# Kernel tuning notes

Measured on AMD Instinct MI355X. Metric: run time of the kernel, lower is better.

Reference implementation:

```python
import jax, jax.numpy as jnp
import numpy as np

H = 32        # query heads
KV = 8        # kv heads (GQA)
D = 128       # head_dim
HID = 4096    # hidden_size
T = 2048      # tokens (single causal sequence)
THETA = 10000.0


def setup_inputs() -> dict:
    key = jax.random.key(0)
    k1, k2, k3 = jax.random.split(key, 3)
    return {
        "positions": jnp.arange(T, dtype=jnp.int32),
        "hidden_states": jax.random.normal(k1, (T, HID), dtype=jnp.float32),
        "w_qkv": jax.random.normal(k2, ((H + 2 * KV) * D, HID), dtype=jnp.float32) * 0.02,
        "w_o": jax.random.normal(k3, (HID, H * D), dtype=jnp.float32) * 0.02,
    }


def _rope_neox(x, cos, sin):
    # x: [T, h, D]; cos/sin: [T, D/2]
    half = x.shape[-1] // 2
    x1, x2 = x[..., :half], x[..., half:]
    c, s = cos[:, None, :], sin[:, None, :]
    return jnp.concatenate([x1 * c - x2 * s, x2 * c + x1 * s], axis=-1)


def reference(positions, hidden_states, w_qkv, w_o):
    t = hidden_states.shape[0]
    qkv = hidden_states @ w_qkv.T                      # [T, (H+2KV)*D]
    q, k, v = jnp.split(qkv, [H * D, H * D + KV * D], axis=-1)
    q = q.reshape(t, H, D)
    k = k.reshape(t, KV, D)
    v = v.reshape(t, KV, D)

    # neox-style RoPE over full head_dim
    half = D // 2
    inv_freq = 1.0 / (THETA ** (jnp.arange(0, D, 2, dtype=jnp.float32) / D))  # [D/2]
    freqs = positions.astype(jnp.float32)[:, None] * inv_freq                 # [T, D/2]
    cos, sin = jnp.cos(freqs), jnp.sin(freqs)
    q = _rope_neox(q, cos, sin)
    k = _rope_neox(k, cos, sin)

    # GQA: expand kv heads to match query heads
    rep = H // KV
    k = jnp.repeat(k, rep, axis=1)                     # [T, H, D]
    v = jnp.repeat(v, rep, axis=1)

    scale = D ** -0.5
    scores = jnp.einsum('thd,shd->hts', q, k) * scale  # [H, T, T]
    causal = positions[:, None] >= positions[None, :]  # [T, T]
    neg = jnp.finfo(scores.dtype).min
    scores = jnp.where(causal[None], scores, neg)
    attn = jax.nn.softmax(scores, axis=-1)
    out = jnp.einsum('hts,shd->thd', attn, v).reshape(t, H * D)
    return out @ w_o.T                                 # [T, HID]
```

## Files before the change

### kernel.cpp

```cpp
#include <hip/hip_runtime.h>
#include <hip/hip_bf16.h>
#include <cstdint>

typedef __bf16 bf16;
typedef __bf16 bf16x8 __attribute__((ext_vector_type(8)));
typedef float f32x4 __attribute__((ext_vector_type(4)));

#define DEV __device__ __forceinline__

DEV f32x4 mfma16(bf16x8 a, bf16x8 b, f32x4 c) {
  return __builtin_amdgcn_mfma_f32_16x16x32_bf16(a, b, c, 0, 0, 0);
}

DEV void gl2lds16(const void* g, void* l) {
  __builtin_amdgcn_global_load_lds((__attribute__((address_space(1))) void*)g,
                                   (__attribute__((address_space(3))) void*)l,
                                   16, 0, 0);
}

DEV void cvt8(const float* __restrict__ s, bf16* __restrict__ d) {
  f32x4 a = *(const f32x4*)(s);
  f32x4 b = *(const f32x4*)(s + 4);
  bf16x8 o;
#pragma unroll
  for (int e = 0; e < 4; ++e) { o[e] = (bf16)a[e]; o[e + 4] = (bf16)b[e]; }
  *(bf16x8*)(d) = o;
}

__global__ void cvt3(const float* __restrict__ s0, bf16* __restrict__ d0, int n0,
                     const float* __restrict__ s1, bf16* __restrict__ d1, int n1,
                     const float* __restrict__ s2, bf16* __restrict__ d2) {
  long i = ((long)blockIdx.x * 256 + threadIdx.x) * 8;
  if (i < n0) { cvt8(s0 + i, d0 + i); return; }
  i -= n0;
  if (i < n1) { cvt8(s1 + i, d1 + i); return; }
  i -= n1;
  cvt8(s2 + i, d2 + i);
}

template <typename OutT>
__global__ __launch_bounds__(256) void gemm_bt(const bf16* __restrict__ A,
                                               const bf16* __restrict__ B,
                                               OutT* __restrict__ C,
                                               int M, int N, int K) {
  __shared__ bf16 As[128 * 32];
  __shared__ bf16 Bs[128 * 32];
  const int tid = threadIdx.x;
  const int lane = tid & 63, w = tid >> 6;
  const int wm = w & 1, wn = w >> 1;
  const int quad = lane >> 4, r = lane & 15;
  const long mBase = (long)blockIdx.y * 128, nBase = (long)blockIdx.x * 128;
  f32x4 acc[4][4];
#pragma unroll
  for (int i = 0; i < 4; ++i)
#pragma unroll
    for (int j = 0; j < 4; ++j) acc[i][j] = f32x4{0.f, 0.f, 0.f, 0.f};

  for (int k0 = 0; k0 < K; k0 += 32) {
    __syncthreads();
#pragma unroll
    for (int j = 0; j < 2; ++j) {
      const int c = w * 128 + j * 64 + lane;
      const int row = c >> 2, kc = c & 3;
      const int kcx = kc ^ (row & 3);
      gl2lds16(A + (mBase + row) * (long)K + k0 + kcx * 8,
               (char*)As + (w * 128 + j * 64) * 16);
      gl2lds16(B + (nBase + row) * (long)K + k0 + kcx * 8,
               (char*)Bs + (w * 128 + j * 64) * 16);
    }
    __syncthreads();
    bf16x8 af[4], bfr[4];
#pragma unroll
    for (int i = 0; i < 4; ++i) {
      af[i]  = *(const bf16x8*)(&As[(wm * 64 + i * 16 + r) * 32 + ((quad ^ (r & 3)) << 3)]);
      bfr[i] = *(const bf16x8*)(&Bs[(wn * 64 + i * 16 + r) * 32 + ((quad ^ (r & 3)) << 3)]);
    }
#pragma unroll
    for (int mi = 0; mi < 4; ++mi)
#pragma unroll
      for (int ni = 0; ni < 4; ++ni)
        acc[mi][ni] = mfma16(af[mi], bfr[ni], acc[mi][ni]);
  }
#pragma unroll
  for (int mi = 0; mi < 4; ++mi)
#pragma unroll
    for (int ni = 0; ni < 4; ++ni)
#pragma unroll
      for (int rg = 0; rg < 4; ++rg) {
        long row = mBase + wm * 64 + mi * 16 + quad * 4 + rg;
        long col = nBase + wn * 64 + ni * 16 + r;
        C[row * N + col] = (OutT)acc[mi][ni][rg];
      }
}

__global__ void rope_kernel(bf16* __restrict__ qkv, const int* __restrict__ pos) {
  int idx = blockIdx.x * 256 + threadIdx.x;
  int g = idx & 7;
  int rest = idx >> 3;
  int head = rest % 40;
  int t = rest / 40;
  bf16* p = qkv + (long)t * 6144 + head * 128 + g * 8;
  bf16x8 a = *(const bf16x8*)(p);
  bf16x8 b = *(const bf16x8*)(p + 64);
  const float pf = (float)pos[t];
  bf16x8 oa, ob;
#pragma unroll
  for (int e = 0; e < 8; ++e) {
    const int d = g * 8 + e;
    const float invf = __builtin_expf(-(float)d * (9.210340371976184f / 64.0f));
    const float fr = pf * invf;
    const float c = __builtin_cosf(fr), s = __builtin_sinf(fr);
    const float x1 = (float)a[e], x2 = (float)b[e];
    oa[e] = (bf16)(x1 * c - x2 * s);
    ob[e] = (bf16)(x2 * c + x1 * s);
  }
  *(bf16x8*)(p) = oa;
  *(bf16x8*)(p + 64) = ob;
}

__global__ __launch_bounds__(256, 2) void attn_kernel(const bf16* __restrict__ qkv,
                                                      bf16* __restrict__ out) {
  constexpr int LDV = 72, LDP = 72;
  constexpr float SCL2 = 0.08838834764831845f * 1.4426950408889634f;
  __shared__ bf16 Ks[64 * 128];
  __shared__ bf16 Vt[128 * LDV];
  __shared__ bf16 Ps[64 * LDP];
  const int tid = threadIdx.x;
  const int lane = tid & 63, w = tid >> 6;
  const int quad = lane >> 4, r = lane & 15;
  const int pr = blockIdx.x, h = blockIdx.y;
  const int kvh = h >> 2;

  bf16x8 kreg[4], vreg[4];
  int srow[4], sdc[4];
#pragma unroll
  for (int ii = 0; ii < 4; ++ii) {
    const int c = ii * 256 + tid;
    srow[ii] = c >> 4;
    sdc[ii] = c & 15;
  }

  for (int which = 0; which < 2; ++which) {
    const int qt = which ? (31 - pr) : pr;
    const int rowq = qt * 64 + w * 16;

    bf16x8 qf[4];
#pragma unroll
    for (int ks = 0; ks < 4; ++ks)
      qf[ks] = *(const bf16x8*)(qkv + (long)(rowq + r) * 6144 + h * 128 + ks * 32 + quad * 8);

    f32x4 of[8];
#pragma unroll
    for (int di = 0; di < 8; ++di) of[di] = f32x4{0.f, 0.f, 0.f, 0.f};
    float mrun[4], lrun[4];
#pragma unroll
    for (int rg = 0; rg < 4; ++rg) { mrun[rg] = -__builtin_inff(); lrun[rg] = 0.f; }

    const int ntiles = qt + 1;
#pragma unroll
    for (int ii = 0; ii < 4; ++ii) {
      const long rb = (long)srow[ii] * 6144 + kvh * 128;
      kreg[ii] = *(const bf16x8*)(qkv + rb + 4096 + sdc[ii] * 8);
      vreg[ii] = *(const bf16x8*)(qkv + rb + 5120 + sdc[ii] * 8);
    }

    for (int kt = 0; kt < ntiles; ++kt) {
      const int kvbase = kt * 64;
      __syncthreads();
#pragma unroll
      for (int ii = 0; ii < 4; ++ii) {
        const int row = srow[ii], dc = sdc[ii];
        *(bf16x8*)(&Ks[row * 128 + ((dc ^ (row & 15)) << 3)]) = kreg[ii];
        const int pc = (((row >> 3) ^ (dc & 7)) << 3) + (row & 7);
#pragma unroll
        for (int e = 0; e < 8; ++e) Vt[(dc * 8 + e) * LDV + pc] = vreg[ii][e];
      }
      __syncthreads();
      {
        const int kvn = (kt + 1 < ntiles) ? (kt + 1) * 64 : kt * 64;
#pragma unroll
        for (int ii = 0; ii < 4; ++ii) {
          const long rb = (long)(kvn + srow[ii]) * 6144 + kvh * 128;
          kreg[ii] = *(const bf16x8*)(qkv + rb + 4096 + sdc[ii] * 8);
          vreg[ii] = *(const bf16x8*)(qkv + rb + 5120 + sdc[ii] * 8);
        }
      }

      f32x4 sacc[4];
#pragma unroll
      for (int ni = 0; ni < 4; ++ni) sacc[ni] = f32x4{0.f, 0.f, 0.f, 0.f};
#pragma unroll
      for (int ks = 0; ks < 4; ++ks) {
        bf16x8 kf[4];
#pragma unroll
        for (int ni = 0; ni < 4; ++ni)
          kf[ni] = *(const bf16x8*)(&Ks[(ni * 16 + r) * 128 + (((ks * 4 + quad) ^ r) << 3)]);
#pragma unroll
        for (int ni = 0; ni < 4; ++ni) sacc[ni] = mfma16(qf[ks], kf[ni], sacc[ni]);
      }

      float mt[4];
#pragma unroll
      for (int rg = 0; rg < 4; ++rg) mt[rg] = -1e30f;
      if (kt == qt) {
        const int rq = rowq + quad * 4;
#pragma unroll
        for (int ni = 0; ni < 4; ++ni) {
          const int ck = kvbase + ni * 16 + r;
#pragma unroll
          for (int rg = 0; rg < 4; ++rg) {
            float sv = sacc[ni][rg];
            sv = (ck > rq + rg) ? -1e30f : sv;
            sacc[ni][rg] = sv;
            mt[rg] = fmaxf(mt[rg], sv);
          }
        }
      } else {
#pragma unroll
        for (int ni = 0; ni < 4; ++ni)
#pragma unroll
          for (int rg = 0; rg < 4; ++rg) mt[rg] = fmaxf(mt[rg], sacc[ni][rg]);
      }
#pragma unroll
      for (int rg = 0; rg < 4; ++rg) {
        float v = mt[rg];
        v = fmaxf(v, __shfl_xor(v, 1));
        v = fmaxf(v, __shfl_xor(v, 2));
        v = fmaxf(v, __shfl_xor(v, 4));
        v = fmaxf(v, __shfl_xor(v, 8));
        mt[rg] = v;
      }
      float alpha[4], rsum[4];
#pragma unroll
      for (int rg = 0; rg < 4; ++rg) {
        const float mnew = fmaxf(mrun[rg], mt[rg]);
        alpha[rg] = __builtin_exp2f((mrun[rg] - mnew) * SCL2);
        mrun[rg] = mnew;
        rsum[rg] = 0.f;
      }
#pragma unroll
      for (int ni = 0; ni < 4; ++ni)
#pragma unroll
        for (int rg = 0; rg < 4; ++rg) {
          const float pv = __builtin_exp2f((sacc[ni][rg] - mrun[rg]) * SCL2);
          rsum[rg] += pv;
          Ps[(w * 16 + quad * 4 + rg) * LDP + ni * 16 + r] = (bf16)pv;
        }
#pragma unroll
      for (int rg = 0; rg < 4; ++rg) {
        float v = rsum[rg];
        v += __shfl_xor(v, 1);
        v += __shfl_xor(v, 2);
        v += __shfl_xor(v, 4);
        v += __shfl_xor(v, 8);
        lrun[rg] = lrun[rg] * alpha[rg] + v;
      }
#pragma unroll
      for (int di = 0; di < 8; ++di)
#pragma unroll
        for (int rg = 0; rg < 4; ++rg) of[di][rg] *= alpha[rg];

#pragma unroll
      for (int js = 0; js < 2; ++js) {
        const bf16x8 pf = *(const bf16x8*)(&Ps[(w * 16 + r) * LDP + js * 32 + quad * 8]);
#pragma unroll
        for (int di = 0; di < 8; ++di) {
          const int vrow = di * 16 + r;
          const int vcol = (((js * 4 + quad) ^ ((vrow >> 3) & 7)) << 3);
          const bf16x8 vf = *(const bf16x8*)(&Vt[vrow * LDV + vcol]);
          of[di] = mfma16(pf, vf, of[di]);
        }
      }
    }

#pragma unroll
    for (int rg = 0; rg < 4; ++rg) {
      const float inv = 1.f / lrun[rg];
      const long t = rowq + quad * 4 + rg;
#pragma unroll
      for (int di = 0; di < 8; ++di)
        out[t * 4096 + h * 128 + di * 16 + r] = (bf16)(of[di][rg] * inv);
    }
  }
}

extern "C" void kernel_launch(void* const* d_in, const int* in_sizes, int n_in,
                              void* d_out, int out_size, void* d_ws, size_t ws_size,
                              hipStream_t stream) {
  const int* positions = (const int*)d_in[0];
  const float* hidden = (const float*)d_in[1];
  const float* w_qkv = (const float*)d_in[2];
  const float* w_o = (const float*)d_in[3];
  float* out = (float*)d_out;

  char* ws = (char*)d_ws;
  bf16* hid_b  = (bf16*)(ws);
  bf16* wqkv_b = (bf16*)(ws + 16777216);
  bf16* wo_b   = (bf16*)(ws + 67108864);
  bf16* qkv    = (bf16*)(ws + 100663296);
  bf16* attn   = (bf16*)(ws + 125829120);

  cvt3<<<24576, 256, 0, stream>>>(hidden, hid_b, 8388608,
                                  w_qkv, wqkv_b, 25165824,
                                  w_o, wo_b);
  gemm_bt<bf16><<<dim3(48, 16), 256, 0, stream>>>(hid_b, wqkv_b, qkv, 2048, 6144, 4096);
  rope_kernel<<<2560, 256, 0, stream>>>(qkv, positions);
  attn_kernel<<<dim3(16, 32), 256, 0, stream>>>(qkv, attn);
  gemm_bt<float><<<dim3(32, 16), 256, 0, stream>>>(attn, wo_b, out, 2048, 4096, 4096);
}
```

Before: 573.4 us.

## Split-K output GEMM with atomics, double-buffer attention K/V, drop GEMM LDS swizzle

The output projection GEMM is split along K into two halves across blockIdx.z, accumulating with float atomicAdd into a zeroed output, to double the block count. The attention kernel double-buffers K and V in LDS, removing one barrier per tile. The GEMM's XOR swizzle on LDS loads and reads is removed, which may add bank conflicts. The atomics add a memset and nondeterministic summation order.

```diff
diff --git a/kernel.cpp b/kernel.cpp
--- a/kernel.cpp
+++ b/kernel.cpp
@@ -38,7 +38,7 @@
   cvt8(s2 + i, d2 + i);
 }
 
-template <typename OutT>
+template <typename OutT, int SPLIT>
 __global__ __launch_bounds__(256) void gemm_bt(const bf16* __restrict__ A,
                                                const bf16* __restrict__ B,
                                                OutT* __restrict__ C,
@@ -50,30 +50,31 @@
   const int wm = w & 1, wn = w >> 1;
   const int quad = lane >> 4, r = lane & 15;
   const long mBase = (long)blockIdx.y * 128, nBase = (long)blockIdx.x * 128;
+  const int Kh = K / SPLIT;
+  const int kBeg = blockIdx.z * Kh, kEnd = kBeg + Kh;
   f32x4 acc[4][4];
 #pragma unroll
   for (int i = 0; i < 4; ++i)
 #pragma unroll
     for (int j = 0; j < 4; ++j) acc[i][j] = f32x4{0.f, 0.f, 0.f, 0.f};
 
-  for (int k0 = 0; k0 < K; k0 += 32) {
+  for (int k0 = kBeg; k0 < kEnd; k0 += 32) {
     __syncthreads();
 #pragma unroll
     for (int j = 0; j < 2; ++j) {
       const int c = w * 128 + j * 64 + lane;
       const int row = c >> 2, kc = c & 3;
-      const int kcx = kc ^ (row & 3);
-      gl2lds16(A + (mBase + row) * (long)K + k0 + kcx * 8,
+      gl2lds16(A + (mBase + row) * (long)K + k0 + kc * 8,
                (char*)As + (w * 128 + j * 64) * 16);
-      gl2lds16(B + (nBase + row) * (long)K + k0 + kcx * 8,
+      gl2lds16(B + (nBase + row) * (long)K + k0 + kc * 8,
                (char*)Bs + (w * 128 + j * 64) * 16);
     }
     __syncthreads();
     bf16x8 af[4], bfr[4];
 #pragma unroll
     for (int i = 0; i < 4; ++i) {
-      af[i]  = *(const bf16x8*)(&As[(wm * 64 + i * 16 + r) * 32 + ((quad ^ (r & 3)) << 3)]);
-      bfr[i] = *(const bf16x8*)(&Bs[(wn * 64 + i * 16 + r) * 32 + ((quad ^ (r & 3)) << 3)]);
+      af[i]  = *(const bf16x8*)(&As[(wm * 64 + i * 16 + r) * 32 + quad * 8]);
+      bfr[i] = *(const bf16x8*)(&Bs[(wn * 64 + i * 16 + r) * 32 + quad * 8]);
     }
 #pragma unroll
     for (int mi = 0; mi < 4; ++mi)
@@ -89,7 +90,10 @@
       for (int rg = 0; rg < 4; ++rg) {
         long row = mBase + wm * 64 + mi * 16 + quad * 4 + rg;
         long col = nBase + wn * 64 + ni * 16 + r;
-        C[row * N + col] = (OutT)acc[mi][ni][rg];
+        if (SPLIT > 1)
+          atomicAdd((float*)&C[row * N + col], acc[mi][ni][rg]);
+        else
+          C[row * N + col] = (OutT)acc[mi][ni][rg];
       }
 }
 
@@ -122,8 +126,8 @@
                                                       bf16* __restrict__ out) {
   constexpr int LDV = 72, LDP = 72;
   constexpr float SCL2 = 0.08838834764831845f * 1.4426950408889634f;
-  __shared__ bf16 Ks[64 * 128];
-  __shared__ bf16 Vt[128 * LDV];
+  __shared__ bf16 Ks[2][64 * 128];
+  __shared__ bf16 Vt[2][128 * LDV];
   __shared__ bf16 Ps[64 * LDP];
   const int tid = threadIdx.x;
   const int lane = tid & 63, w = tid >> 6;
@@ -166,16 +170,15 @@
 
     for (int kt = 0; kt < ntiles; ++kt) {
       const int kvbase = kt * 64;
-      __syncthreads();
+      const int buf = kt & 1;
 #pragma unroll
       for (int ii = 0; ii < 4; ++ii) {
         const int row = srow[ii], dc = sdc[ii];
-        *(bf16x8*)(&Ks[row * 128 + ((dc ^ (row & 15)) << 3)]) = kreg[ii];
+        *(bf16x8*)(&Ks[buf][row * 128 + ((dc ^ (row & 15)) << 3)]) = kreg[ii];
         const int pc = (((row >> 3) ^ (dc & 7)) << 3) + (row & 7);
 #pragma unroll
-        for (int e = 0; e < 8; ++e) Vt[(dc * 8 + e) * LDV + pc] = vreg[ii][e];
-      }
-      __syncthreads();
+        for (int e = 0; e < 8; ++e) Vt[buf][(dc * 8 + e) * LDV + pc] = vreg[ii][e];
+      }
       {
         const int kvn = (kt + 1 < ntiles) ? (kt + 1) * 64 : kt * 64;
 #pragma unroll
@@ -185,6 +188,7 @@
           vreg[ii] = *(const bf16x8*)(qkv + rb + 5120 + sdc[ii] * 8);
         }
       }
+      __syncthreads();
 
       f32x4 sacc[4];
 #pragma unroll
@@ -194,7 +198,7 @@
         bf16x8 kf[4];
 #pragma unroll
         for (int ni = 0; ni < 4; ++ni)
-          kf[ni] = *(const bf16x8*)(&Ks[(ni * 16 + r) * 128 + (((ks * 4 + quad) ^ r) << 3)]);
+          kf[ni] = *(const bf16x8*)(&Ks[buf][(ni * 16 + r) * 128 + (((ks * 4 + quad) ^ r) << 3)]);
 #pragma unroll
         for (int ni = 0; ni < 4; ++ni) sacc[ni] = mfma16(qf[ks], kf[ni], sacc[ni]);
       }
@@ -267,7 +271,7 @@
         for (int di = 0; di < 8; ++di) {
           const int vrow = di * 16 + r;
           const int vcol = (((js * 4 + quad) ^ ((vrow >> 3) & 7)) << 3);
-          const bf16x8 vf = *(const bf16x8*)(&Vt[vrow * LDV + vcol]);
+          const bf16x8 vf = *(const bf16x8*)(&Vt[buf][vrow * LDV + vcol]);
           of[di] = mfma16(pf, vf, of[di]);
         }
       }
@@ -303,8 +307,9 @@
   cvt3<<<24576, 256, 0, stream>>>(hidden, hid_b, 8388608,
                                   w_qkv, wqkv_b, 25165824,
                                   w_o, wo_b);
-  gemm_bt<bf16><<<dim3(48, 16), 256, 0, stream>>>(hid_b, wqkv_b, qkv, 2048, 6144, 4096);
+  gemm_bt<bf16, 1><<<dim3(48, 16), 256, 0, stream>>>(hid_b, wqkv_b, qkv, 2048, 6144, 4096);
   rope_kernel<<<2560, 256, 0, stream>>>(qkv, positions);
   attn_kernel<<<dim3(16, 32), 256, 0, stream>>>(qkv, attn);
-  gemm_bt<float><<<dim3(32, 16), 256, 0, stream>>>(attn, wo_b, out, 2048, 4096, 4096);
-}
+  hipMemsetAsync(d_out, 0, (size_t)out_size * sizeof(float), stream);
+  gemm_bt<float, 2><<<dim3(32, 16, 2), 256, 0, stream>>>(attn, wo_b, out, 2048, 4096, 4096);
+}
```

New measurement: 608.1 us. +6.0%, slower.
